# Kernel optimization log

Hardware: AMD Instinct MI355X
Metric: run time of the kernel (lower is better)

## Reference

```python
import jax, jax.numpy as jnp
import numpy as np

B, D, H, W, C = 1, 16, 56, 56, 128
NH = 4
WD, WH, WW = 8, 7, 7          # window size (t, h, w)
SD, SH, SW = 4, 3, 3          # shift size
N = WD * WH * WW              # tokens per window = 392
HEAD = C // NH
SCALE = HEAD ** -0.5
HID = 4 * C                   # mlp_ratio = 4
REL_TAB = (2 * WD - 1) * (2 * WH - 1) * (2 * WW - 1)


def _rel_pos_index():
    coords = np.stack(np.meshgrid(np.arange(WD), np.arange(WH), np.arange(WW), indexing='ij'))
    cf = coords.reshape(3, -1)
    rel = (cf[:, :, None] - cf[:, None, :]).transpose(1, 2, 0).astype(np.int64)
    rel[..., 0] += WD - 1; rel[..., 1] += WH - 1; rel[..., 2] += WW - 1
    rel[..., 0] *= (2 * WH - 1) * (2 * WW - 1)
    rel[..., 1] *= (2 * WW - 1)
    return rel.sum(-1)  # (N, N)

REL_IDX = jnp.asarray(_rel_pos_index())


def _win_part_np(x):
    b, d, h, w, c = x.shape
    x = x.reshape(b, d // WD, WD, h // WH, WH, w // WW, WW, c)
    return x.transpose(0, 1, 3, 5, 2, 4, 6, 7).reshape(-1, N, c)


def _attn_mask():
    # shifted-window mask, computed once on host (static)
    img = np.zeros((1, D, H, W, 1))
    cnt = 0
    for ds in (slice(0, -WD), slice(-WD, -SD), slice(-SD, None)):
        for hs in (slice(0, -WH), slice(-WH, -SH), slice(-SH, None)):
            for ws in (slice(0, -WW), slice(-WW, -SW), slice(-SW, None)):
                img[:, ds, hs, ws, :] = cnt
                cnt += 1
    mw = _win_part_np(img).reshape(-1, N)
    am = mw[:, None, :] - mw[:, :, None]
    return np.where(am != 0, -100.0, 0.0).astype(np.float32)  # (nW, N, N)

ATTN_MASK = jnp.asarray(_attn_mask())


def layer_norm(x, w, b, eps=1e-5):
    mu = x.mean(-1, keepdims=True)
    var = ((x - mu) ** 2).mean(-1, keepdims=True)
    return (x - mu) * jax.lax.rsqrt(var + eps) * w + b


def window_partition(x):
    b = x.shape[0]
    x = x.reshape(b, D // WD, WD, H // WH, WH, W // WW, WW, C)
    return x.transpose(0, 1, 3, 5, 2, 4, 6, 7).reshape(-1, N, C)


def window_reverse(win, b):
    x = win.reshape(b, D // WD, H // WH, W // WW, WD, WH, WW, C)
    return x.transpose(0, 1, 4, 2, 5, 3, 6, 7).reshape(b, D, H, W, C)


def setup_inputs() -> dict:
    key = jax.random.key(0)
    ks = jax.random.split(key, 16)
    s = 0.02
    return {
        'x': jax.random.normal(ks[0], (B, D, H, W, C), jnp.float32),
        'norm1_w': jnp.ones((C,), jnp.float32),
        'norm1_b': jnp.zeros((C,), jnp.float32),
        'qkv_w': jax.random.normal(ks[1], (3 * C, C), jnp.float32) * s,
        'qkv_b': jnp.zeros((3 * C,), jnp.float32),
        'rel_pos_table': jax.random.normal(ks[2], (REL_TAB, NH), jnp.float32) * s,
        'proj_w': jax.random.normal(ks[3], (C, C), jnp.float32) * s,
        'proj_b': jnp.zeros((C,), jnp.float32),
        'norm2_w': jnp.ones((C,), jnp.float32),
        'norm2_b': jnp.zeros((C,), jnp.float32),
        'fc1_w': jax.random.normal(ks[4], (HID, C), jnp.float32) * s,
        'fc1_b': jnp.zeros((HID,), jnp.float32),
        'fc2_w': jax.random.normal(ks[5], (C, HID), jnp.float32) * s,
        'fc2_b': jnp.zeros((C,), jnp.float32),
    }


def reference(x, norm1_w, norm1_b, qkv_w, qkv_b, rel_pos_table, proj_w, proj_b,
              norm2_w, norm2_b, fc1_w, fc1_b, fc2_w, fc2_b):
    shortcut = x
    h = layer_norm(x, norm1_w, norm1_b)
    # cyclic shift
    h = jnp.roll(h, shift=(-SD, -SH, -SW), axis=(1, 2, 3))
    win = window_partition(h)                      # (B*nW, N, C)
    Bw = win.shape[0]
    qkv = win @ qkv_w.T + qkv_b                    # (Bw, N, 3C)
    qkv = qkv.reshape(Bw, N, 3, NH, HEAD).transpose(2, 0, 3, 1, 4)
    q, k, v = qkv[0] * SCALE, qkv[1], qkv[2]       # (Bw, NH, N, HEAD)
    bias = rel_pos_table[REL_IDX].transpose(2, 0, 1)  # (NH, N, N)
    A = jnp.einsum('bhnc,bhmc->bhnm', q, k) + bias[None]
    nW = Bw // B
    A = A.reshape(B, nW, NH, N, N) + ATTN_MASK[None, :, None]
    A = jax.nn.softmax(A.reshape(Bw, NH, N, N), axis=-1)
    y = jnp.einsum('bhnm,bhmc->bhnc', A, v).transpose(0, 2, 1, 3).reshape(Bw, N, C)
    y = y @ proj_w.T + proj_b
    h = window_reverse(y, B)
    h = jnp.roll(h, shift=(SD, SH, SW), axis=(1, 2, 3))
    x = shortcut + h
    # Mlp module: internal LayerNorm + residual (see Mlp.forward_fn)
    m = layer_norm(x, norm2_w, norm2_b)
    m = jax.nn.gelu(m @ fc1_w.T + fc1_b, approximate=False)
    m = m @ fc2_w.T + fc2_b
    return x + m
```

## Files before the change

### kernel.cpp

```cpp
#include <hip/hip_runtime.h>
#include <hip/hip_bf16.h>
#include <math.h>


typedef short s16x8 __attribute__((ext_vector_type(8)));
typedef unsigned short u16x8 __attribute__((ext_vector_type(8)));
typedef float fp32x4 __attribute__((ext_vector_type(4)));

#define T_TOT 50176
#define N_TOK 392
#define N_WIN 128

__device__ __forceinline__ unsigned short f2bf(float f) {
    union { float f; unsigned u; } v; v.f = f;
    unsigned r = v.u + 0x7FFFu + ((v.u >> 16) & 1u);
    return (unsigned short)(r >> 16);
}
__device__ __forceinline__ float bf2f(unsigned short u) {
    union { unsigned u; float f; } v; v.u = ((unsigned)u) << 16;
    return v.f;
}

__global__ void cvt_w_k(const float* __restrict__ wq, const float* __restrict__ wp,
                        const float* __restrict__ w1, const float* __restrict__ w2,
                        unsigned short* __restrict__ oq, unsigned short* __restrict__ op,
                        unsigned short* __restrict__ o1, unsigned short* __restrict__ o2)
{
    int i = blockIdx.x * 256 + threadIdx.x;
    if (i < 384 * 128) oq[i] = f2bf(wq[i]);
    if (i < 128 * 128) op[i] = f2bf(wp[i]);
    if (i < 512 * 128) { o1[i] = f2bf(w1[i]); o2[i] = f2bf(w2[i]); }
}

__global__ void bias_tab_k(const float* __restrict__ tab, float* __restrict__ out)
{
    int idx = blockIdx.x * 256 + threadIdx.x;
    if (idx >= 4 * N_TOK * N_TOK) return;
    int h = idx / (N_TOK * N_TOK), r = idx % (N_TOK * N_TOK);
    int i = r / N_TOK, j = r % N_TOK;
    int di = i / 49, hi = (i % 49) / 7, wi = i % 7;
    int dj = j / 49, hj = (j % 49) / 7, wj = j % 7;
    int rel = (di - dj + 7) * 169 + (hi - hj + 6) * 13 + (wi - wj + 6);
    out[idx] = tab[rel * 4 + h];
}

__global__ __launch_bounds__(256) void ln1_part_k(
    const float* __restrict__ x, const float* __restrict__ w,
    const float* __restrict__ b, unsigned short* __restrict__ xw)
{
    const int t = blockIdx.x * 4 + (threadIdx.x >> 6);
    const int lane = threadIdx.x & 63;
    const int win = t / N_TOK, n = t % N_TOK;
    const int wd = win >> 6, wh = (win >> 3) & 7, ww = win & 7;
    const int td = n / 49, rr = n % 49, th = rr / 7, tw = rr % 7;
    const int gd = wd * 8 + td, gh = wh * 7 + th, gw = ww * 7 + tw;
    const int sd = (gd + 4) & 15;
    int sh = gh + 3; if (sh >= 56) sh -= 56;
    int sw = gw + 3; if (sw >= 56) sw -= 56;
    const float* px = x + (((size_t)sd * 56 + sh) * 56 + sw) * 128;
    float v0 = px[lane], v1 = px[lane + 64];
    float s = v0 + v1, s2 = v0 * v0 + v1 * v1;
#pragma unroll
    for (int o = 32; o > 0; o >>= 1) { s += __shfl_xor(s, o); s2 += __shfl_xor(s2, o); }
    float mu = s * (1.f / 128.f);
    float var = s2 * (1.f / 128.f) - mu * mu;
    float rstd = rsqrtf(var + 1e-5f);
    unsigned short* po = xw + (size_t)t * 128;
    po[lane]      = f2bf((v0 - mu) * rstd * w[lane]      + b[lane]);
    po[lane + 64] = f2bf((v1 - mu) * rstd * w[lane + 64] + b[lane + 64]);
}

__global__ __launch_bounds__(256) void ln2_k(
    const float* __restrict__ x1, const float* __restrict__ w,
    const float* __restrict__ b, unsigned short* __restrict__ xn)
{
    const int t = blockIdx.x * 4 + (threadIdx.x >> 6);
    const int lane = threadIdx.x & 63;
    const float* px = x1 + (size_t)t * 128;
    float v0 = px[lane], v1 = px[lane + 64];
    float s = v0 + v1, s2 = v0 * v0 + v1 * v1;
#pragma unroll
    for (int o = 32; o > 0; o >>= 1) { s += __shfl_xor(s, o); s2 += __shfl_xor(s2, o); }
    float mu = s * (1.f / 128.f);
    float var = s2 * (1.f / 128.f) - mu * mu;
    float rstd = rsqrtf(var + 1e-5f);
    unsigned short* po = xn + (size_t)t * 128;
    po[lane]      = f2bf((v0 - mu) * rstd * w[lane]      + b[lane]);
    po[lane + 64] = f2bf((v1 - mu) * rstd * w[lane + 64] + b[lane + 64]);
}

template<int K, int EPI>
__global__ __launch_bounds__(256, 2) void gemm_k(
    const unsigned short* __restrict__ A,
    const unsigned short* __restrict__ Bt,
    const float* __restrict__ bias,
    const float* __restrict__ resid,
    void* __restrict__ outp)
{
    __shared__ __align__(16) unsigned short Asl[128 * 64];
    __shared__ __align__(16) unsigned short Bsl[128 * 64];
    const int bm = blockIdx.x * 128;
    const int bn = blockIdx.y * 128;
    const int tid = threadIdx.x;
    const int lane = tid & 63;
    const int wave = tid >> 6;
    const int wr = wave >> 1, wc = wave & 1;
    const int lr = lane & 15;
    const int lk = (lane >> 4) << 3;

    fp32x4 acc[4][4];
#pragma unroll
    for (int i = 0; i < 4; ++i)
#pragma unroll
        for (int j = 0; j < 4; ++j) acc[i][j] = {0.f, 0.f, 0.f, 0.f};

    for (int ks = 0; ks < K; ks += 64) {
        __syncthreads();
#pragma unroll
        for (int it = 0; it < 4; ++it) {
            int chunk = it * 256 + tid;
            int row = chunk >> 3;
            int kc = (chunk & 7) << 3;
            *(uint4*)&Asl[row * 64 + kc] =
                *(const uint4*)&A[(size_t)(bm + row) * K + ks + kc];
            *(uint4*)&Bsl[row * 64 + kc] =
                *(const uint4*)&Bt[(size_t)(bn + row) * K + ks + kc];
        }
        __syncthreads();
#pragma unroll
        for (int kk = 0; kk < 64; kk += 32) {
            s16x8 af[4], bfr[4];
#pragma unroll
            for (int mb = 0; mb < 4; ++mb)
                af[mb] = *(const s16x8*)&Asl[(wr * 64 + mb * 16 + lr) * 64 + kk + lk];
#pragma unroll
            for (int nb = 0; nb < 4; ++nb)
                bfr[nb] = *(const s16x8*)&Bsl[(wc * 64 + nb * 16 + lr) * 64 + kk + lk];
#pragma unroll
            for (int mb = 0; mb < 4; ++mb)
#pragma unroll
                for (int nb = 0; nb < 4; ++nb)
                    acc[mb][nb] = __builtin_amdgcn_mfma_f32_16x16x32_bf16(
                        af[mb], bfr[nb], acc[mb][nb], 0, 0, 0);
        }
    }

    const int crow = (lane >> 4) << 2;
    const int ccol = lane & 15;
#pragma unroll
    for (int mb = 0; mb < 4; ++mb) {
#pragma unroll
        for (int nb = 0; nb < 4; ++nb) {
#pragma unroll
            for (int r = 0; r < 4; ++r) {
                const int grow = bm + wr * 64 + mb * 16 + crow + r;
                const int gcol = bn + wc * 64 + nb * 16 + ccol;
                float v = acc[mb][nb][r] + bias[gcol];
                if (EPI == 0) {
                    if (gcol < 128) v *= 0.17677669529663687f;
                    ((unsigned short*)outp)[(size_t)grow * 384 + gcol] = f2bf(v);
                } else if (EPI == 1) {
                    int w  = grow / N_TOK, n = grow % N_TOK;
                    int wd = w >> 6, wh = (w >> 3) & 7, ww = w & 7;
                    int td = n / 49, rr = n % 49, th = rr / 7, tw = rr % 7;
                    int gd = wd * 8 + td, gh = wh * 7 + th, gw = ww * 7 + tw;
                    int sd = (gd + 4) & 15;
                    int sh = gh + 3; if (sh >= 56) sh -= 56;
                    int sw = gw + 3; if (sw >= 56) sw -= 56;
                    size_t oi = (((size_t)sd * 56 + sh) * 56 + sw) * 128 + gcol;
                    ((float*)outp)[oi] = v + resid[oi];
                } else if (EPI == 2) {
                    v = 0.5f * v * (1.f + erff(v * 0.70710678118654752f));
                    ((unsigned short*)outp)[(size_t)grow * 512 + gcol] = f2bf(v);
                } else {
                    size_t oi = (size_t)grow * 128 + gcol;
                    ((float*)outp)[oi] = v + resid[oi];
                }
            }
        }
    }
}

#define KSTR 40
#define VSTR 424
#define PSTR 424

__global__ __launch_bounds__(256, 1) void attn_k(
    const unsigned short* __restrict__ qkv,
    const float* __restrict__ btab,
    unsigned short* __restrict__ y)
{
    __shared__ __align__(16) unsigned short Ksh[416 * KSTR];
    __shared__ __align__(16) unsigned short Vt[32 * VSTR];
    __shared__ __align__(16) unsigned short Psh[4][16 * PSTR];
    __shared__ unsigned char rid_sh[416];

    const int blk = blockIdx.x;
    const int wI = blk >> 2, h = blk & 3;
    const int tid = threadIdx.x;
    const int wave = tid >> 6, lane = tid & 63;
    const int lr = lane & 15, g = lane >> 4, lk = g << 3;
    const unsigned short* base = qkv + (size_t)wI * N_TOK * 384;

    const int wd = wI >> 6, wh = (wI >> 3) & 7, ww = wI & 7;
    const bool boundary = (wd == 1) | (wh == 7) | (ww == 7);

    for (int idx = tid; idx < 392 * 4; idx += 256) {
        int j = idx >> 2, c0 = (idx & 3) << 3;
        *(uint4*)&Ksh[j * KSTR + c0] =
            *(const uint4*)&base[(size_t)j * 384 + 128 + h * 32 + c0];
    }
    for (int idx = tid; idx < 24 * 4; idx += 256) {
        int j = 392 + (idx >> 2), c0 = (idx & 3) << 3;
        u16x8 z = {};
        *(u16x8*)&Ksh[j * KSTR + c0] = z;
    }
    for (int idx = tid; idx < 32 * 49; idx += 256) {
        int c = idx & 31, j0 = (idx >> 5) << 3;
        const unsigned short* vp = base + 256 + h * 32 + c;
        u16x8 tmp;
#pragma unroll
        for (int i = 0; i < 8; ++i) tmp[i] = vp[(size_t)(j0 + i) * 384];
        *(u16x8*)&Vt[c * VSTR + j0] = tmp;
    }
    for (int idx = tid; idx < 32 * 3; idx += 256) {
        int c = idx & 31, j0 = 392 + ((idx >> 5) << 3);
        u16x8 z = {};
        *(u16x8*)&Vt[c * VSTR + j0] = z;
    }
    for (int n = tid; n < 416; n += 256) {
        int nn = (n < 392) ? n : 391;
        int td = nn / 49, rr = nn % 49, th = rr / 7, tw = rr % 7;
        int gd = wd * 8 + td, gh = wh * 7 + th, gw = ww * 7 + tw;
        int r = ((gd < 8) ? 0 : ((gd < 12) ? 9 : 18)) +
                ((gh < 49) ? 0 : ((gh < 53) ? 3 : 6)) +
                ((gw < 49) ? 0 : ((gw < 53) ? 1 : 2));
        rid_sh[n] = (unsigned char)r;
    }
    __syncthreads();

    const float* bb = btab + (size_t)h * N_TOK * N_TOK;
    unsigned short* pw = &Psh[wave][0];

    for (int rt = wave; rt < 25; rt += 4) {
        const int qrow = (rt * 16 + lr < 392) ? rt * 16 + lr : 391;
        s16x8 aq = *(const s16x8*)&base[(size_t)qrow * 384 + h * 32 + lk];
        fp32x4 acc[26];
#pragma unroll
        for (int ct = 0; ct < 26; ++ct) {
            s16x8 bk = *(const s16x8*)&Ksh[(ct * 16 + lr) * KSTR + lk];
            fp32x4 z = {0.f, 0.f, 0.f, 0.f};
            acc[ct] = __builtin_amdgcn_mfma_f32_16x16x32_bf16(aq, bk, z, 0, 0, 0);
        }
        const int i0 = rt * 16 + (g << 2);
        unsigned char ri[4];
        int ic[4];
#pragma unroll
        for (int r = 0; r < 4; ++r) {
            ic[r] = (i0 + r < 392) ? i0 + r : 391;
            ri[r] = rid_sh[ic[r]];
        }
        float mx[4] = {-1e30f, -1e30f, -1e30f, -1e30f};
#pragma unroll
        for (int ct = 0; ct < 26; ++ct) {
            int j = ct * 16 + lr;
            bool jv = j < 392;
            int jc = jv ? j : 391;
            unsigned char rj = rid_sh[jc];
#pragma unroll
            for (int r = 0; r < 4; ++r) {
                float s = acc[ct][r] + bb[(size_t)ic[r] * N_TOK + jc];
                if (boundary && (ri[r] != rj)) s -= 100.f;
                if (!jv) s = -1e30f;
                acc[ct][r] = s;
                mx[r] = fmaxf(mx[r], s);
            }
        }
#pragma unroll
        for (int r = 0; r < 4; ++r)
#pragma unroll
            for (int m = 1; m < 16; m <<= 1)
                mx[r] = fmaxf(mx[r], __shfl_xor(mx[r], m));
        float sum[4] = {0.f, 0.f, 0.f, 0.f};
#pragma unroll
        for (int ct = 0; ct < 26; ++ct)
#pragma unroll
            for (int r = 0; r < 4; ++r) {
                float p = __expf(acc[ct][r] - mx[r]);
                acc[ct][r] = p;
                sum[r] += p;
            }
#pragma unroll
        for (int r = 0; r < 4; ++r) {
#pragma unroll
            for (int m = 1; m < 16; m <<= 1) sum[r] += __shfl_xor(sum[r], m);
            sum[r] = 1.f / sum[r];
        }
#pragma unroll
        for (int ct = 0; ct < 26; ++ct)
#pragma unroll
            for (int r = 0; r < 4; ++r)
                pw[((g << 2) + r) * PSTR + ct * 16 + lr] = f2bf(acc[ct][r] * sum[r]);
        fp32x4 o0 = {0.f, 0.f, 0.f, 0.f}, o1 = {0.f, 0.f, 0.f, 0.f};
#pragma unroll
        for (int ks = 0; ks < 13; ++ks) {
            s16x8 ap  = *(const s16x8*)&pw[lr * PSTR + ks * 32 + lk];
            s16x8 bv0 = *(const s16x8*)&Vt[lr * VSTR + ks * 32 + lk];
            s16x8 bv1 = *(const s16x8*)&Vt[(16 + lr) * VSTR + ks * 32 + lk];
            o0 = __builtin_amdgcn_mfma_f32_16x16x32_bf16(ap, bv0, o0, 0, 0, 0);
            o1 = __builtin_amdgcn_mfma_f32_16x16x32_bf16(ap, bv1, o1, 0, 0, 0);
        }
#pragma unroll
        for (int r = 0; r < 4; ++r) {
            int row = rt * 16 + (g << 2) + r;
            if (row < 392) {
                size_t ob = ((size_t)wI * N_TOK + row) * 128 + h * 32;
                y[ob + lr]      = f2bf(o0[r]);
                y[ob + 16 + lr] = f2bf(o1[r]);
            }
        }
    }
}

extern "C" void kernel_launch(void* const* d_in, const int* in_sizes, int n_in,
                              void* d_out, int out_size, void* d_ws, size_t ws_size,
                              hipStream_t stream)
{
    const float* x      = (const float*)d_in[0];
    const float* n1w    = (const float*)d_in[1];
    const float* n1b    = (const float*)d_in[2];
    const float* qkv_w  = (const float*)d_in[3];
    const float* qkv_b  = (const float*)d_in[4];
    const float* rpt    = (const float*)d_in[5];
    const float* proj_w = (const float*)d_in[6];
    const float* proj_b = (const float*)d_in[7];
    const float* n2w    = (const float*)d_in[8];
    const float* n2b    = (const float*)d_in[9];
    const float* fc1_w  = (const float*)d_in[10];
    const float* fc1_b  = (const float*)d_in[11];
    const float* fc2_w  = (const float*)d_in[12];
    const float* fc2_b  = (const float*)d_in[13];

    char* ws = (char*)d_ws;
    unsigned short* xw  = (unsigned short*)(ws);
    unsigned short* qkv = (unsigned short*)(ws + 12845056);
    unsigned short* y   = (unsigned short*)(ws + 51380224);
    float*          x1  = (float*)         (ws + 64225280);
    unsigned short* xn  = (unsigned short*)(ws + 89915392);
    unsigned short* hid = (unsigned short*)(ws + 102760448);
    unsigned short* wq  = (unsigned short*)(ws + 154140672);
    unsigned short* wp  = (unsigned short*)(ws + 154238976);
    unsigned short* w1  = (unsigned short*)(ws + 154271744);
    unsigned short* w2  = (unsigned short*)(ws + 154402816);
    float*          bt  = (float*)         (ws + 154533888);

    hipLaunchKernelGGL(cvt_w_k, dim3(256), dim3(256), 0, stream,
                       qkv_w, proj_w, fc1_w, fc2_w, wq, wp, w1, w2);
    hipLaunchKernelGGL(bias_tab_k, dim3((4 * N_TOK * N_TOK + 255) / 256), dim3(256),
                       0, stream, rpt, bt);
    hipLaunchKernelGGL(ln1_part_k, dim3(T_TOT / 4), dim3(256), 0, stream,
                       x, n1w, n1b, xw);
    hipLaunchKernelGGL((gemm_k<128, 0>), dim3(392, 3), dim3(256), 0, stream,
                       xw, wq, qkv_b, (const float*)nullptr, (void*)qkv);
    hipLaunchKernelGGL(attn_k, dim3(512), dim3(256), 0, stream, qkv, bt, y);
    hipLaunchKernelGGL((gemm_k<128, 1>), dim3(392, 1), dim3(256), 0, stream,
                       y, wp, proj_b, x, (void*)x1);
    hipLaunchKernelGGL(ln2_k, dim3(T_TOT / 4), dim3(256), 0, stream,
                       x1, n2w, n2b, xn);
    hipLaunchKernelGGL((gemm_k<128, 2>), dim3(392, 4), dim3(256), 0, stream,
                       xn, w1, fc1_b, (const float*)nullptr, (void*)hid);
    hipLaunchKernelGGL((gemm_k<512, 3>), dim3(392, 1), dim3(256), 0, stream,
                       hid, w2, fc2_b, x1, d_out);
}
```

Before: 302.9 us.

## Transpose attention score tiles so each lane owns one query row

The QK^T MFMA operands are swapped so each lane holds scores for a single query row across four consecutive keys. This allows float4 bias loads and packed region-id loads, and reduces the softmax max/sum to two cross-lane shuffles. Probabilities are now converted and written into a small per-wave transposed P tile one k-step at a time, instead of a full 16x424 buffer, and normalization is deferred to the output. The column loop drops to 25 tiles, and launch bounds are raised to allow two blocks per CU, which cuts LDS use but adds register pressure.

Measured after the change: 257.2 us. -15.1%, faster.

```diff
diff --git a/kernel.cpp b/kernel.cpp
--- a/kernel.cpp
+++ b/kernel.cpp
@@ -183,17 +183,17 @@
 
 #define KSTR 40
 #define VSTR 424
-#define PSTR 424
-
-__global__ __launch_bounds__(256, 1) void attn_k(
+#define PTS  40
+
+__global__ __launch_bounds__(256, 2) void attn_k(
     const unsigned short* __restrict__ qkv,
     const float* __restrict__ btab,
     unsigned short* __restrict__ y)
 {
     __shared__ __align__(16) unsigned short Ksh[416 * KSTR];
     __shared__ __align__(16) unsigned short Vt[32 * VSTR];
-    __shared__ __align__(16) unsigned short Psh[4][16 * PSTR];
-    __shared__ unsigned char rid_sh[416];
+    __shared__ __align__(16) unsigned short Pt[4][16 * PTS];
+    __shared__ __align__(4) unsigned char rid_sh[416];
 
     const int blk = blockIdx.x;
     const int wI = blk >> 2, h = blk & 3;
@@ -240,71 +240,89 @@
     __syncthreads();
 
     const float* bb = btab + (size_t)h * N_TOK * N_TOK;
-    unsigned short* pw = &Psh[wave][0];
+    unsigned short* pw = &Pt[wave][0];
+    const int j0 = g << 2;
 
     for (int rt = wave; rt < 25; rt += 4) {
-        const int qrow = (rt * 16 + lr < 392) ? rt * 16 + lr : 391;
-        s16x8 aq = *(const s16x8*)&base[(size_t)qrow * 384 + h * 32 + lk];
-        fp32x4 acc[26];
-#pragma unroll
-        for (int ct = 0; ct < 26; ++ct) {
-            s16x8 bk = *(const s16x8*)&Ksh[(ct * 16 + lr) * KSTR + lk];
+        const int irow = rt * 16 + lr;
+        const int ic = (irow < 392) ? irow : 391;
+        s16x8 bq = *(const s16x8*)&base[(size_t)ic * 384 + h * 32 + lk];
+        fp32x4 acc[25];
+#pragma unroll
+        for (int ct = 0; ct < 25; ++ct) {
+            s16x8 ak = *(const s16x8*)&Ksh[(ct * 16 + lr) * KSTR + lk];
             fp32x4 z = {0.f, 0.f, 0.f, 0.f};
-            acc[ct] = __builtin_amdgcn_mfma_f32_16x16x32_bf16(aq, bk, z, 0, 0, 0);
-        }
-        const int i0 = rt * 16 + (g << 2);
-        unsigned char ri[4];
-        int ic[4];
-#pragma unroll
-        for (int r = 0; r < 4; ++r) {
-            ic[r] = (i0 + r < 392) ? i0 + r : 391;
-            ri[r] = rid_sh[ic[r]];
-        }
-        float mx[4] = {-1e30f, -1e30f, -1e30f, -1e30f};
-#pragma unroll
-        for (int ct = 0; ct < 26; ++ct) {
-            int j = ct * 16 + lr;
-            bool jv = j < 392;
-            int jc = jv ? j : 391;
-            unsigned char rj = rid_sh[jc];
+            acc[ct] = __builtin_amdgcn_mfma_f32_16x16x32_bf16(ak, bq, z, 0, 0, 0);
+        }
+        const int ri = rid_sh[ic];
+        float mx = -1e30f;
+#pragma unroll
+        for (int ct = 0; ct < 24; ++ct) {
+            float4 bv = *(const float4*)&bb[(size_t)ic * N_TOK + ct * 16 + j0];
+            unsigned rj4 = *(const unsigned*)&rid_sh[ct * 16 + j0];
+            const float bs[4] = {bv.x, bv.y, bv.z, bv.w};
 #pragma unroll
             for (int r = 0; r < 4; ++r) {
-                float s = acc[ct][r] + bb[(size_t)ic[r] * N_TOK + jc];
-                if (boundary && (ri[r] != rj)) s -= 100.f;
-                if (!jv) s = -1e30f;
+                float s = acc[ct][r] + bs[r];
+                int rj = (rj4 >> (8 * r)) & 255;
+                if (boundary && rj != ri) s -= 100.f;
                 acc[ct][r] = s;
-                mx[r] = fmaxf(mx[r], s);
-            }
-        }
-#pragma unroll
-        for (int r = 0; r < 4; ++r)
-#pragma unroll
-            for (int m = 1; m < 16; m <<= 1)
-                mx[r] = fmaxf(mx[r], __shfl_xor(mx[r], m));
-        float sum[4] = {0.f, 0.f, 0.f, 0.f};
-#pragma unroll
-        for (int ct = 0; ct < 26; ++ct)
+                mx = fmaxf(mx, s);
+            }
+        }
+        {
+            float4 bv = {0.f, 0.f, 0.f, 0.f};
+            unsigned rj4 = 0;
+            if (g < 2) {
+                bv = *(const float4*)&bb[(size_t)ic * N_TOK + 384 + j0];
+                rj4 = *(const unsigned*)&rid_sh[384 + j0];
+            }
+            const float bs[4] = {bv.x, bv.y, bv.z, bv.w};
 #pragma unroll
             for (int r = 0; r < 4; ++r) {
-                float p = __expf(acc[ct][r] - mx[r]);
+                float s = -1e30f;
+                if (g < 2) {
+                    s = acc[24][r] + bs[r];
+                    int rj = (rj4 >> (8 * r)) & 255;
+                    if (boundary && rj != ri) s -= 100.f;
+                }
+                acc[24][r] = s;
+                mx = fmaxf(mx, s);
+            }
+        }
+        mx = fmaxf(mx, __shfl_xor(mx, 16));
+        mx = fmaxf(mx, __shfl_xor(mx, 32));
+        float sum = 0.f;
+#pragma unroll
+        for (int ct = 0; ct < 25; ++ct)
+#pragma unroll
+            for (int r = 0; r < 4; ++r) {
+                float p = __expf(acc[ct][r] - mx);
                 acc[ct][r] = p;
-                sum[r] += p;
-            }
-#pragma unroll
-        for (int r = 0; r < 4; ++r) {
-#pragma unroll
-            for (int m = 1; m < 16; m <<= 1) sum[r] += __shfl_xor(sum[r], m);
-            sum[r] = 1.f / sum[r];
-        }
-#pragma unroll
-        for (int ct = 0; ct < 26; ++ct)
-#pragma unroll
-            for (int r = 0; r < 4; ++r)
-                pw[((g << 2) + r) * PSTR + ct * 16 + lr] = f2bf(acc[ct][r] * sum[r]);
+                sum += p;
+            }
+        sum += __shfl_xor(sum, 16);
+        sum += __shfl_xor(sum, 32);
+        const float rs = 1.f / sum;
         fp32x4 o0 = {0.f, 0.f, 0.f, 0.f}, o1 = {0.f, 0.f, 0.f, 0.f};
 #pragma unroll
         for (int ks = 0; ks < 13; ++ks) {
-            s16x8 ap  = *(const s16x8*)&pw[lr * PSTR + ks * 32 + lk];
+            unsigned w0, w1, w2 = 0, w3 = 0;
+            asm("v_cvt_pk_bf16_f32 %0, %1, %2"
+                : "=v"(w0) : "v"(acc[2 * ks][0]), "v"(acc[2 * ks][1]));
+            asm("v_cvt_pk_bf16_f32 %0, %1, %2"
+                : "=v"(w1) : "v"(acc[2 * ks][2]), "v"(acc[2 * ks][3]));
+            if (ks < 12) {
+                asm("v_cvt_pk_bf16_f32 %0, %1, %2"
+                    : "=v"(w2) : "v"(acc[2 * ks + 1][0]), "v"(acc[2 * ks + 1][1]));
+                asm("v_cvt_pk_bf16_f32 %0, %1, %2"
+                    : "=v"(w3) : "v"(acc[2 * ks + 1][2]), "v"(acc[2 * ks + 1][3]));
+            }
+            *(unsigned*)&pw[lr * PTS + j0]          = w0;
+            *(unsigned*)&pw[lr * PTS + j0 + 2]      = w1;
+            *(unsigned*)&pw[lr * PTS + 16 + j0]     = w2;
+            *(unsigned*)&pw[lr * PTS + 16 + j0 + 2] = w3;
+            s16x8 ap  = *(const s16x8*)&pw[lr * PTS + lk];
             s16x8 bv0 = *(const s16x8*)&Vt[lr * VSTR + ks * 32 + lk];
             s16x8 bv1 = *(const s16x8*)&Vt[(16 + lr) * VSTR + ks * 32 + lk];
             o0 = __builtin_amdgcn_mfma_f32_16x16x32_bf16(ap, bv0, o0, 0, 0, 0);
@@ -312,11 +330,12 @@
         }
 #pragma unroll
         for (int r = 0; r < 4; ++r) {
-            int row = rt * 16 + (g << 2) + r;
+            const float rsr = __shfl(rs, (g << 2) + r);
+            const int row = rt * 16 + (g << 2) + r;
             if (row < 392) {
                 size_t ob = ((size_t)wI * N_TOK + row) * 128 + h * 32;
-                y[ob + lr]      = f2bf(o0[r]);
-                y[ob + 16 + lr] = f2bf(o1[r]);
+                y[ob + lr]      = f2bf(o0[r] * rsr);
+                y[ob + 16 + lr] = f2bf(o1[r] * rsr);
             }
         }
     }
```
